# Kernel tuning notes

Measured on AMD Instinct MI355X. Metric: run time of the kernel, lower is better.

The kernel has to match this reference:

```python
import jax, jax.numpy as jnp
import numpy as np

H = 16        # num attention heads
KV = 4        # num key/value heads (GQA)
HD = 128      # head dim
CAP = 50.0    # attn_logits_soft_cap
SCALE = HD ** -0.5
ROPE_THETA = 10000.0


def rotate_half(x):
    return jnp.concatenate([-x[..., HD // 2:], x[..., :HD // 2]], axis=-1)


def setup_inputs() -> dict:
    key = jax.random.key(0)
    k0, k1, k2, k3, k4 = jax.random.split(key, 5)
    B, S, D = 2, 2048, 2048
    hidden_states = jax.random.normal(k0, (B, S, D), dtype=jnp.float32)
    # real rotary tables (HF apply_rotary_pos_emb convention: emb = cat(freqs, freqs))
    pos = jnp.arange(S, dtype=jnp.float32)
    inv_freq = 1.0 / (ROPE_THETA ** (jnp.arange(0, HD, 2, dtype=jnp.float32) / HD))
    freqs = pos[:, None] * inv_freq[None, :]          # [S, HD/2]
    emb = jnp.concatenate([freqs, freqs], axis=-1)    # [S, HD]
    cos = jnp.broadcast_to(jnp.cos(emb)[None], (B, S, HD)).astype(jnp.float32)
    sin = jnp.broadcast_to(jnp.sin(emb)[None], (B, S, HD)).astype(jnp.float32)
    Wq = 0.02 * jax.random.normal(k1, (H * HD, D), dtype=jnp.float32)
    Wk = 0.02 * jax.random.normal(k2, (KV * HD, D), dtype=jnp.float32)
    Wv = 0.02 * jax.random.normal(k3, (KV * HD, D), dtype=jnp.float32)
    Wo = 0.02 * jax.random.normal(k4, (D, H * HD), dtype=jnp.float32)
    return {"hidden_states": hidden_states, "cos": cos, "sin": sin,
            "Wq": Wq, "Wk": Wk, "Wv": Wv, "Wo": Wo}


def reference(hidden_states, cos, sin, Wq, Wk, Wv, Wo):
    B, S, D = hidden_states.shape
    # QKV projections (HF Linear: y = x @ W.T)
    q = jnp.einsum('bsd,hd->bsh', hidden_states, Wq).reshape(B, S, H, HD).transpose(0, 2, 1, 3)
    k = jnp.einsum('bsd,hd->bsh', hidden_states, Wk).reshape(B, S, KV, HD).transpose(0, 2, 1, 3)
    v = jnp.einsum('bsd,hd->bsh', hidden_states, Wv).reshape(B, S, KV, HD).transpose(0, 2, 1, 3)
    # RoPE
    cosb = cos[:, None, :, :]  # [B,1,S,HD]
    sinb = sin[:, None, :, :]
    q = q * cosb + rotate_half(q) * sinb
    k = k * cosb + rotate_half(k) * sinb
    # GQA: repeat kv heads
    rep = H // KV
    k = jnp.repeat(k, rep, axis=1)  # [B,H,S,HD]
    v = jnp.repeat(v, rep, axis=1)
    # splash attention == causal attention with tanh logits soft cap
    scores = jnp.einsum('bhqd,bhkd->bhqk', q * SCALE, k)
    scores = CAP * jnp.tanh(scores / CAP)
    causal = jnp.tril(jnp.ones((S, S), dtype=bool))
    scores = jnp.where(causal[None, None], scores, jnp.float32(-1e30))
    attn = jax.nn.softmax(scores, axis=-1)
    out = jnp.einsum('bhqk,bhkd->bhqd', attn, v)
    out = out.transpose(0, 2, 1, 3).reshape(B, S, H * HD)
    return jnp.einsum('bsh,dh->bsd', out, Wo)
```

## Files before the change

### kernel.cpp

```cpp
#include <hip/hip_runtime.h>
#include <hip/hip_bf16.h>
#include <stdint.h>

typedef __bf16 bf16x8 __attribute__((ext_vector_type(8)));
typedef float f32x4 __attribute__((ext_vector_type(4)));
typedef float f32x16 __attribute__((ext_vector_type(16)));

#define NB_H 16
#define NB_KV 4
#define NB_HD 128
#define NB_B 2
#define NB_S 2048
#define NB_D 2048
#define NB_M (NB_B*NB_S)
#define NB_NQKV 3072
#define CAPF 50.0f
#define SCALEF 0.08838834764831845f

__device__ __forceinline__ ushort f2bf(float x){
  uint32_t u = __float_as_uint(x);
  u += 0x7fffu + ((u >> 16) & 1u);
  return (ushort)(u >> 16);
}
__device__ __forceinline__ float bf2f(ushort u){
  return __uint_as_float(((uint32_t)u) << 16);
}
__device__ __forceinline__ void gload_lds16(const void* g, void* l){
  __builtin_amdgcn_global_load_lds(
      (const __attribute__((address_space(1))) uint32_t*)g,
      (__attribute__((address_space(3))) uint32_t*)l, 16, 0, 0);
}

__global__ __launch_bounds__(256) void cvt_all(const float* __restrict__ hs,
                                               const float* __restrict__ wq,
                                               const float* __restrict__ wk,
                                               const float* __restrict__ wv,
                                               const float* __restrict__ wo,
                                               ushort* __restrict__ hsb,
                                               ushort* __restrict__ wqkv,
                                               ushort* __restrict__ wob){
  int q = blockIdx.x * blockDim.x + threadIdx.x;
  const float* src; ushort* dst; int i;
  if (q < 2097152)      { src = hs; dst = hsb;            i = q; }
  else if (q < 3145728) { src = wq; dst = wqkv;           i = q - 2097152; }
  else if (q < 3407872) { src = wk; dst = wqkv + 4194304; i = q - 3145728; }
  else if (q < 3670016) { src = wv; dst = wqkv + 5242880; i = q - 3407872; }
  else                  { src = wo; dst = wob;            i = q - 3670016; }
  float4 v = ((const float4*)src)[i];
  ushort4 o;
  o.x = f2bf(v.x); o.y = f2bf(v.y); o.z = f2bf(v.z); o.w = f2bf(v.w);
  ((ushort4*)dst)[i] = o;
}

__global__ __launch_bounds__(256) void gemm_bt(const ushort* __restrict__ A,
                                               const ushort* __restrict__ Bw,
                                               ushort* __restrict__ Cb,
                                               float* __restrict__ Cf,
                                               int M, int N, int K, int nbx){
  int nwg = gridDim.x;
  int cpx = nwg >> 3;
  int wg = blockIdx.x;
  int swz = (wg & 7) * cpx + (wg >> 3);
  int bx = swz % nbx, by = swz / nbx;

  __shared__ ushort As[128 * 32];
  __shared__ ushort Bs[128 * 32];
  int tid = threadIdx.x;
  int w = tid >> 6, l = tid & 63;
  int lr = l & 15, lk = l >> 4;
  int row0 = by * 128, col0 = bx * 128;
  int wm = w >> 1, wn = w & 1;

  f32x4 acc[4][4];
#pragma unroll
  for (int mi = 0; mi < 4; ++mi)
#pragma unroll
    for (int nj = 0; nj < 4; ++nj)
      acc[mi][nj] = f32x4{0.f, 0.f, 0.f, 0.f};

  for (int k0 = 0; k0 < K; k0 += 32) {
#pragma unroll
    for (int c = 0; c < 2; ++c) {
      int off = w * 2048 + c * 1024 + l * 16;
      int r = off >> 6;
      int cb = off & 63;
      gload_lds16(A + (size_t)(row0 + r) * K + k0 + (cb >> 1), (char*)As + off);
      gload_lds16(Bw + (size_t)(col0 + r) * K + k0 + (cb >> 1), (char*)Bs + off);
    }
    __syncthreads();
    bf16x8 af[4], bfr[4];
#pragma unroll
    for (int mi = 0; mi < 4; ++mi)
      af[mi] = *(const bf16x8*)(As + (wm * 64 + mi * 16 + lr) * 32 + lk * 8);
#pragma unroll
    for (int nj = 0; nj < 4; ++nj)
      bfr[nj] = *(const bf16x8*)(Bs + (wn * 64 + nj * 16 + lr) * 32 + lk * 8);
    __builtin_amdgcn_s_setprio(1);
#pragma unroll
    for (int mi = 0; mi < 4; ++mi)
#pragma unroll
      for (int nj = 0; nj < 4; ++nj)
        acc[mi][nj] = __builtin_amdgcn_mfma_f32_16x16x32_bf16(af[mi], bfr[nj], acc[mi][nj], 0, 0, 0);
    __builtin_amdgcn_s_setprio(0);
    __syncthreads();
  }

#pragma unroll
  for (int mi = 0; mi < 4; ++mi)
#pragma unroll
    for (int nj = 0; nj < 4; ++nj)
#pragma unroll
      for (int i = 0; i < 4; ++i) {
        int r = row0 + wm * 64 + mi * 16 + lk * 4 + i;
        int c = col0 + wn * 64 + nj * 16 + lr;
        float v = acc[mi][nj][i];
        if (Cb) Cb[(size_t)r * N + c] = f2bf(v);
        else    Cf[(size_t)r * N + c] = v;
      }
}

__global__ __launch_bounds__(256) void rope_kernel(ushort* __restrict__ qkv,
                                                   const float* __restrict__ cosb,
                                                   const float* __restrict__ sinb){
  int idx = blockIdx.x * blockDim.x + threadIdx.x;
  if (idx >= NB_M * 20 * 64) return;
  int row = idx / 1280;
  int rem = idx - row * 1280;
  int head = rem >> 6;
  int d = rem & 63;
  size_t base = (size_t)row * NB_NQKV + head * 128 + d;
  float a = bf2f(qkv[base]);
  float b = bf2f(qkv[base + 64]);
  float c = cosb[row * 128 + d];
  float s = sinb[row * 128 + d];
  qkv[base]      = f2bf(a * c - b * s);
  qkv[base + 64] = f2bf(b * c + a * s);
}

__global__ __launch_bounds__(256) void vtrans_kernel(const ushort* __restrict__ qkv,
                                                     ushort* __restrict__ vt){
  __shared__ ushort tile[64 * 136];
  int bid = blockIdx.x;
  int s0 = (bid & 31) * 64;
  int kvh = (bid >> 5) & 3;
  int b = bid >> 7;
  int tid = threadIdx.x;
#pragma unroll
  for (int i = 0; i < 4; ++i) {
    int g = tid + i * 256;
    int r = g >> 4, c = g & 15;
    *(uint4*)(tile + r * 136 + c * 8) =
        *(const uint4*)(qkv + (size_t)(b * NB_S + s0 + r) * NB_NQKV + 2560 + kvh * 128 + c * 8);
  }
  __syncthreads();
#pragma unroll
  for (int i = 0; i < 4; ++i) {
    int g = tid + i * 256;
    int dd = g >> 3, c = g & 7;
    union { ushort u[8]; uint4 v; } tmp;
#pragma unroll
    for (int j = 0; j < 8; ++j) tmp.u[j] = tile[(c * 8 + j) * 136 + dd];
    *(uint4*)(vt + ((size_t)(b * NB_KV + kvh) * NB_HD + dd) * NB_S + s0 + c * 8) = tmp.v;
  }
}

__global__ __launch_bounds__(128, 4) void attn_kernel(const ushort* __restrict__ qkv,
                                                      const ushort* __restrict__ vt,
                                                      ushort* __restrict__ obuf){
  __shared__ float accbuf[4096];
  __shared__ float lbuf[64];
  __shared__ ushort trbuf[32 * 140];
  const int tid = threadIdx.x;
  const int w = tid >> 6, l = tid & 63;
  const int ql = l & 31, hi = l >> 5;
  const int blk = blockIdx.x;
  const int g = blk & 7;
  const int inner = blk >> 3;
  const int h_lo = inner & 3;
  const int qtile = 63 - (inner >> 2);
  const int b = g >> 2, kvh = g & 3;
  const int h = kvh * 4 + h_lo;
  const int q0 = qtile * 32;
  const int q = q0 + ql;
  const int nkt = (q0 + 95) >> 6;

  const ushort* Kg = qkv + (size_t)b * NB_S * NB_NQKV + 2048 + kvh * 128;
  const ushort* Vg = vt + (size_t)(b * NB_KV + kvh) * NB_HD * NB_S;

  bf16x8 qf[8];
  {
    const ushort* qrow = qkv + (size_t)(b * NB_S + q) * NB_NQKV + h * 128 + hi * 8;
#pragma unroll
    for (int dc = 0; dc < 8; ++dc)
      qf[dc] = *(const bf16x8*)(qrow + dc * 16);
  }

  f32x16 acc[4];
#pragma unroll
  for (int dt = 0; dt < 4; ++dt)
#pragma unroll
    for (int r = 0; r < 16; ++r) acc[dt][r] = 0.f;
  float l_run = 0.f;

  const float K1 = SCALEF / CAPF;
  const float KW = SCALEF * 1.4426950408889634f;

  for (int kt = w; kt < nkt; kt += 2) {
    const int s0 = kt * 64;
    f32x16 st[2];
#pragma unroll
    for (int t = 0; t < 2; ++t) {
#pragma unroll
      for (int r = 0; r < 16; ++r) st[t][r] = 0.f;
      const ushort* krow = Kg + (size_t)(s0 + t * 32 + ql) * NB_NQKV + hi * 8;
#pragma unroll
      for (int dc = 0; dc < 8; ++dc) {
        bf16x8 kf = *(const bf16x8*)(krow + dc * 16);
        st[t] = __builtin_amdgcn_mfma_f32_32x32x16_bf16(kf, qf[dc], st[t], 0, 0, 0);
      }
    }
    const bool full = (s0 + 63 <= q0);
    const int qmb = q - s0 - 4 * hi;
    float p[2][16];
    float rs = 0.f;
#pragma unroll
    for (int t = 0; t < 2; ++t)
#pragma unroll
      for (int r = 0; r < 16; ++r) {
        float s = st[t][r];
        float x = s * K1;
        float x2 = x * x;
        float ww = s * KW;
        float t1 = fmaf(x2, 0.13333334f, -0.33333334f);
        float y = fmaf(ww * x2, t1, ww);
        y = fminf(y, 72.134752f);
        if (!full) {
          const int koff = t * 32 + (r & 3) + 8 * (r >> 2);
          y = (koff <= qmb) ? y : -1e30f;
        }
        float pe = __builtin_amdgcn_exp2f(y);
        p[t][r] = pe;
        rs += pe;
      }
    rs += __shfl_xor(rs, 32);
    l_run += rs;
    union { __bf16 hh16[32]; uint u[16]; } Pk;
#pragma unroll
    for (int t = 0; t < 2; ++t)
#pragma unroll
      for (int r = 0; r < 16; ++r)
        Pk.hh16[t * 16 + r] = (__bf16)p[t][r];
    uint rec[2][2][2];
#pragma unroll
    for (int t = 0; t < 2; ++t)
#pragma unroll
      for (int hh = 0; hh < 2; ++hh)
#pragma unroll
        for (int wb = 0; wb < 2; ++wb) {
          uint send = hi ? Pk.u[t * 8 + 4 * hh + wb] : Pk.u[t * 8 + 4 * hh + 2 + wb];
          rec[t][hh][wb] = __shfl_xor(send, 32);
        }
#pragma unroll
    for (int c = 0; c < 4; ++c) {
      const int t = c >> 1, hh = c & 1;
      union { uint u[4]; bf16x8 v; } pf;
      pf.u[0] = hi ? rec[t][hh][0] : Pk.u[t * 8 + 4 * hh + 0];
      pf.u[1] = hi ? rec[t][hh][1] : Pk.u[t * 8 + 4 * hh + 1];
      pf.u[2] = hi ? Pk.u[t * 8 + 4 * hh + 2] : rec[t][hh][0];
      pf.u[3] = hi ? Pk.u[t * 8 + 4 * hh + 3] : rec[t][hh][1];
#pragma unroll
      for (int dt = 0; dt < 4; ++dt) {
        bf16x8 vf = *(const bf16x8*)(Vg + (size_t)(dt * 32 + ql) * NB_S + s0 + (c * 2 + hi) * 8);
        acc[dt] = __builtin_amdgcn_mfma_f32_32x32x16_bf16(vf, pf.v, acc[dt], 0, 0, 0);
      }
    }
  }

  if (w == 1) {
#pragma unroll
    for (int dt = 0; dt < 4; ++dt)
#pragma unroll
      for (int r = 0; r < 16; ++r)
        accbuf[(dt * 16 + r) * 64 + l] = acc[dt][r];
    lbuf[l] = l_run;
  }
  __syncthreads();
  if (w == 0) {
#pragma unroll
    for (int dt = 0; dt < 4; ++dt)
#pragma unroll
      for (int r = 0; r < 16; ++r)
        acc[dt][r] += accbuf[(dt * 16 + r) * 64 + l];
    l_run += lbuf[l];
    const float inv = __builtin_amdgcn_rcpf(l_run);
#pragma unroll
    for (int dt = 0; dt < 4; ++dt)
#pragma unroll
      for (int gg = 0; gg < 4; ++gg) {
        ushort4 o;
        o.x = f2bf(acc[dt][4 * gg + 0] * inv);
        o.y = f2bf(acc[dt][4 * gg + 1] * inv);
        o.z = f2bf(acc[dt][4 * gg + 2] * inv);
        o.w = f2bf(acc[dt][4 * gg + 3] * inv);
        const int d0 = dt * 32 + gg * 8 + hi * 4;
        *(ushort4*)(trbuf + ql * 140 + d0) = o;
      }
  }
  __syncthreads();
#pragma unroll
  for (int i = 0; i < 4; ++i) {
    const int qr = i * 8 + (tid >> 4);
    const int c = tid & 15;
    uint4 v = *(const uint4*)(trbuf + qr * 140 + c * 8);
    *(uint4*)(obuf + (size_t)(b * NB_S + q0 + qr) * NB_D + h * 128 + c * 8) = v;
  }
}

extern "C" void kernel_launch(void* const* d_in, const int* in_sizes, int n_in,
                              void* d_out, int out_size, void* d_ws, size_t ws_size,
                              hipStream_t stream) {
  const float* hs   = (const float*)d_in[0];
  const float* cosb = (const float*)d_in[1];
  const float* sinb = (const float*)d_in[2];
  const float* Wq   = (const float*)d_in[3];
  const float* Wk   = (const float*)d_in[4];
  const float* Wv   = (const float*)d_in[5];
  const float* Wo   = (const float*)d_in[6];
  float* out = (float*)d_out;
  char* ws = (char*)d_ws;

  ushort* hsb  = (ushort*)(ws + 0);
  ushort* wqkv = (ushort*)(ws + 16777216);
  ushort* wob  = (ushort*)(ws + 29360128);
  ushort* qkvb = (ushort*)(ws + 37748736);
  ushort* vtb  = (ushort*)(ws + 62914560);
  ushort* ob   = (ushort*)(ws + 67108864);

  cvt_all<<<18432, 256, 0, stream>>>(hs, Wq, Wk, Wv, Wo, hsb, wqkv, wob);

  gemm_bt<<<768, 256, 0, stream>>>(hsb, wqkv, qkvb, nullptr, NB_M, NB_NQKV, NB_D, 24);
  rope_kernel<<<(NB_M * 20 * 64 + 255) / 256, 256, 0, stream>>>(qkvb, cosb, sinb);
  vtrans_kernel<<<NB_B * NB_KV * (NB_S / 64), 256, 0, stream>>>(qkvb, vtb);

  attn_kernel<<<2048, 128, 0, stream>>>(qkvb, vtb, ob);

  gemm_bt<<<512, 256, 0, stream>>>(ob, wob, nullptr, out, NB_M, NB_D, NB_D, 16);
}
```

Baseline: 427.2 us.

## Fuse RoPE into K/V fragment repack and Q load; halve attention LDS reduction buffer

Replaces the separate RoPE and V-transpose kernels with one kv_repack kernel. It applies RoPE to K and writes K and V in MFMA-fragment order, so each lane in attention does contiguous 16-byte loads at a fixed stride. RoPE for Q now runs inside the attention kernel when Q is loaded, which removes the full read-modify-write pass over Q. The cross-wave accumulator reduction now goes through half-size LDS in two rounds, which should help occupancy but adds syncs. The s_setprio hints around the GEMM MFMAs are also removed, and the V fragment buffer reuses the hidden-state workspace region.

```diff
diff --git a/kernel.cpp b/kernel.cpp
--- a/kernel.cpp
+++ b/kernel.cpp
@@ -95,13 +95,11 @@
 #pragma unroll
     for (int nj = 0; nj < 4; ++nj)
       bfr[nj] = *(const bf16x8*)(Bs + (wn * 64 + nj * 16 + lr) * 32 + lk * 8);
-    __builtin_amdgcn_s_setprio(1);
 #pragma unroll
     for (int mi = 0; mi < 4; ++mi)
 #pragma unroll
       for (int nj = 0; nj < 4; ++nj)
         acc[mi][nj] = __builtin_amdgcn_mfma_f32_16x16x32_bf16(af[mi], bfr[nj], acc[mi][nj], 0, 0, 0);
-    __builtin_amdgcn_s_setprio(0);
     __syncthreads();
   }
 
@@ -119,55 +117,70 @@
       }
 }
 
-__global__ __launch_bounds__(256) void rope_kernel(ushort* __restrict__ qkv,
-                                                   const float* __restrict__ cosb,
-                                                   const float* __restrict__ sinb){
-  int idx = blockIdx.x * blockDim.x + threadIdx.x;
-  if (idx >= NB_M * 20 * 64) return;
-  int row = idx / 1280;
-  int rem = idx - row * 1280;
-  int head = rem >> 6;
-  int d = rem & 63;
-  size_t base = (size_t)row * NB_NQKV + head * 128 + d;
-  float a = bf2f(qkv[base]);
-  float b = bf2f(qkv[base + 64]);
-  float c = cosb[row * 128 + d];
-  float s = sinb[row * 128 + d];
-  qkv[base]      = f2bf(a * c - b * s);
-  qkv[base + 64] = f2bf(b * c + a * s);
-}
-
-__global__ __launch_bounds__(256) void vtrans_kernel(const ushort* __restrict__ qkv,
-                                                     ushort* __restrict__ vt){
-  __shared__ ushort tile[64 * 136];
-  int bid = blockIdx.x;
-  int s0 = (bid & 31) * 64;
-  int kvh = (bid >> 5) & 3;
-  int b = bid >> 7;
-  int tid = threadIdx.x;
+__global__ __launch_bounds__(256) void kv_repack(const ushort* __restrict__ qkv,
+                                                 const float* __restrict__ cosb,
+                                                 const float* __restrict__ sinb,
+                                                 ushort* __restrict__ Kf,
+                                                 ushort* __restrict__ Vf){
+  __shared__ ushort Ks[64 * 136];
+  __shared__ ushort Vs[64 * 136];
+  const int blk = blockIdx.x;
+  const int kt = blk & 31, kvh = (blk >> 5) & 3, b = blk >> 7;
+  const int s0 = kt * 64;
+  const int tid = threadIdx.x;
+  {
+    const int r = tid >> 2, c0 = tid & 3;
+    const ushort* src = qkv + (size_t)(b * NB_S + s0 + r) * NB_NQKV + kvh * 128;
+#pragma unroll
+    for (int k = 0; k < 4; ++k) {
+      int c = c0 + k * 4;
+      *(uint4*)(Ks + r * 136 + c * 8) = *(const uint4*)(src + 2048 + c * 8);
+      *(uint4*)(Vs + r * 136 + c * 8) = *(const uint4*)(src + 2560 + c * 8);
+    }
+  }
+  __syncthreads();
+  const int w = tid >> 6, l = tid & 63, ql = l & 31, hi = l >> 5;
+  const size_t fbase = (size_t)((b * NB_KV + kvh) * 32 + kt) * 8192;
 #pragma unroll
   for (int i = 0; i < 4; ++i) {
-    int g = tid + i * 256;
-    int r = g >> 4, c = g & 15;
-    *(uint4*)(tile + r * 136 + c * 8) =
-        *(const uint4*)(qkv + (size_t)(b * NB_S + s0 + r) * NB_NQKV + 2560 + kvh * 128 + c * 8);
-  }
-  __syncthreads();
+    const int idx = i * 4 + w;
+    const int t = idx >> 3, dc = idx & 7;
+    const int row = t * 32 + ql;
+    const int d0 = dc * 16 + hi * 8;
+    union { ushort u[8]; uint4 v; } a, p2;
+    a.v  = *(const uint4*)(Ks + row * 136 + d0);
+    p2.v = *(const uint4*)(Ks + row * 136 + (d0 ^ 64));
+    const float* cr = cosb + (size_t)(b * NB_S + s0 + row) * 128 + d0;
+    const float* sr = sinb + (size_t)(b * NB_S + s0 + row) * 128 + d0;
+    const float sgn = (dc < 4) ? -1.f : 1.f;
+    ushort outv[8];
+#pragma unroll
+    for (int j2 = 0; j2 < 8; ++j2) {
+      float kv = bf2f(a.u[j2]), pv = bf2f(p2.u[j2]);
+      outv[j2] = f2bf(fmaf(sgn * pv, sr[j2], kv * cr[j2]));
+    }
+    *(uint4*)(Kf + fbase + ((size_t)idx * 64 + l) * 8) = *(const uint4*)outv;
+  }
 #pragma unroll
   for (int i = 0; i < 4; ++i) {
-    int g = tid + i * 256;
-    int dd = g >> 3, c = g & 7;
-    union { ushort u[8]; uint4 v; } tmp;
-#pragma unroll
-    for (int j = 0; j < 8; ++j) tmp.u[j] = tile[(c * 8 + j) * 136 + dd];
-    *(uint4*)(vt + ((size_t)(b * NB_KV + kvh) * NB_HD + dd) * NB_S + s0 + c * 8) = tmp.v;
+    const int idx = i * 4 + w;
+    const int c = idx >> 2, dt = idx & 3;
+    const int col = dt * 32 + ql;
+    ushort outv[8];
+#pragma unroll
+    for (int j2 = 0; j2 < 8; ++j2)
+      outv[j2] = Vs[((2 * c + hi) * 8 + j2) * 136 + col];
+    *(uint4*)(Vf + fbase + ((size_t)idx * 64 + l) * 8) = *(const uint4*)outv;
   }
 }
 
 __global__ __launch_bounds__(128, 4) void attn_kernel(const ushort* __restrict__ qkv,
-                                                      const ushort* __restrict__ vt,
+                                                      const ushort* __restrict__ Kf,
+                                                      const ushort* __restrict__ Vf,
+                                                      const float* __restrict__ cosb,
+                                                      const float* __restrict__ sinb,
                                                       ushort* __restrict__ obuf){
-  __shared__ float accbuf[4096];
+  __shared__ float accbuf[2048];
   __shared__ float lbuf[64];
   __shared__ ushort trbuf[32 * 140];
   const int tid = threadIdx.x;
@@ -184,15 +197,30 @@
   const int q = q0 + ql;
   const int nkt = (q0 + 95) >> 6;
 
-  const ushort* Kg = qkv + (size_t)b * NB_S * NB_NQKV + 2048 + kvh * 128;
-  const ushort* Vg = vt + (size_t)(b * NB_KV + kvh) * NB_HD * NB_S;
+  const ushort* Kfb = Kf + (size_t)(b * NB_KV + kvh) * 262144 + l * 8;
+  const ushort* Vfb = Vf + (size_t)(b * NB_KV + kvh) * 262144 + l * 8;
 
   bf16x8 qf[8];
   {
-    const ushort* qrow = qkv + (size_t)(b * NB_S + q) * NB_NQKV + h * 128 + hi * 8;
-#pragma unroll
-    for (int dc = 0; dc < 8; ++dc)
-      qf[dc] = *(const bf16x8*)(qrow + dc * 16);
+    const ushort* qrow = qkv + (size_t)(b * NB_S + q) * NB_NQKV + h * 128;
+    const float* cr = cosb + (size_t)(b * NB_S + q) * 128;
+    const float* sr = sinb + (size_t)(b * NB_S + q) * 128;
+#pragma unroll
+    for (int dc = 0; dc < 4; ++dc) {
+      union { ushort u[8]; uint4 v; } lo, hi8;
+      lo.v  = *(const uint4*)(qrow + dc * 16 + hi * 8);
+      hi8.v = *(const uint4*)(qrow + (dc + 4) * 16 + hi * 8);
+      __bf16 o1[8], o2[8];
+#pragma unroll
+      for (int j2 = 0; j2 < 8; ++j2) {
+        const int d1 = dc * 16 + hi * 8 + j2;
+        float a = bf2f(lo.u[j2]), bb = bf2f(hi8.u[j2]);
+        o1[j2] = (__bf16)(a * cr[d1] - bb * sr[d1]);
+        o2[j2] = (__bf16)(bb * cr[d1 + 64] + a * sr[d1 + 64]);
+      }
+      qf[dc]     = *(bf16x8*)o1;
+      qf[dc + 4] = *(bf16x8*)o2;
+    }
   }
 
   f32x16 acc[4];
@@ -207,15 +235,16 @@
 
   for (int kt = w; kt < nkt; kt += 2) {
     const int s0 = kt * 64;
+    const ushort* kp = Kfb + (size_t)kt * 8192;
+    const ushort* vp = Vfb + (size_t)kt * 8192;
     f32x16 st[2];
 #pragma unroll
     for (int t = 0; t < 2; ++t) {
 #pragma unroll
       for (int r = 0; r < 16; ++r) st[t][r] = 0.f;
-      const ushort* krow = Kg + (size_t)(s0 + t * 32 + ql) * NB_NQKV + hi * 8;
 #pragma unroll
       for (int dc = 0; dc < 8; ++dc) {
-        bf16x8 kf = *(const bf16x8*)(krow + dc * 16);
+        bf16x8 kf = *(const bf16x8*)(kp + (t * 8 + dc) * 512);
         st[t] = __builtin_amdgcn_mfma_f32_32x32x16_bf16(kf, qf[dc], st[t], 0, 0, 0);
       }
     }
@@ -270,7 +299,7 @@
       pf.u[3] = hi ? Pk.u[t * 8 + 4 * hh + 3] : rec[t][hh][1];
 #pragma unroll
       for (int dt = 0; dt < 4; ++dt) {
-        bf16x8 vf = *(const bf16x8*)(Vg + (size_t)(dt * 32 + ql) * NB_S + s0 + (c * 2 + hi) * 8);
+        bf16x8 vf = *(const bf16x8*)(vp + (c * 4 + dt) * 512);
         acc[dt] = __builtin_amdgcn_mfma_f32_32x32x16_bf16(vf, pf.v, acc[dt], 0, 0, 0);
       }
     }
@@ -278,7 +307,7 @@
 
   if (w == 1) {
 #pragma unroll
-    for (int dt = 0; dt < 4; ++dt)
+    for (int dt = 0; dt < 2; ++dt)
 #pragma unroll
       for (int r = 0; r < 16; ++r)
         accbuf[(dt * 16 + r) * 64 + l] = acc[dt][r];
@@ -287,11 +316,27 @@
   __syncthreads();
   if (w == 0) {
 #pragma unroll
-    for (int dt = 0; dt < 4; ++dt)
+    for (int dt = 0; dt < 2; ++dt)
 #pragma unroll
       for (int r = 0; r < 16; ++r)
         acc[dt][r] += accbuf[(dt * 16 + r) * 64 + l];
     l_run += lbuf[l];
+  }
+  __syncthreads();
+  if (w == 1) {
+#pragma unroll
+    for (int dt = 0; dt < 2; ++dt)
+#pragma unroll
+      for (int r = 0; r < 16; ++r)
+        accbuf[(dt * 16 + r) * 64 + l] = acc[dt + 2][r];
+  }
+  __syncthreads();
+  if (w == 0) {
+#pragma unroll
+    for (int dt = 0; dt < 2; ++dt)
+#pragma unroll
+      for (int r = 0; r < 16; ++r)
+        acc[dt + 2][r] += accbuf[(dt * 16 + r) * 64 + l];
     const float inv = __builtin_amdgcn_rcpf(l_run);
 #pragma unroll
     for (int dt = 0; dt < 4; ++dt)
@@ -333,16 +378,17 @@
   ushort* wqkv = (ushort*)(ws + 16777216);
   ushort* wob  = (ushort*)(ws + 29360128);
   ushort* qkvb = (ushort*)(ws + 37748736);
-  ushort* vtb  = (ushort*)(ws + 62914560);
+  ushort* kfb  = (ushort*)(ws + 62914560);
   ushort* ob   = (ushort*)(ws + 67108864);
+  ushort* vfb  = (ushort*)(ws + 0);
 
   cvt_all<<<18432, 256, 0, stream>>>(hs, Wq, Wk, Wv, Wo, hsb, wqkv, wob);
 
   gemm_bt<<<768, 256, 0, stream>>>(hsb, wqkv, qkvb, nullptr, NB_M, NB_NQKV, NB_D, 24);
-  rope_kernel<<<(NB_M * 20 * 64 + 255) / 256, 256, 0, stream>>>(qkvb, cosb, sinb);
-  vtrans_kernel<<<NB_B * NB_KV * (NB_S / 64), 256, 0, stream>>>(qkvb, vtb);
-
-  attn_kernel<<<2048, 128, 0, stream>>>(qkvb, vtb, ob);
+
+  kv_repack<<<256, 256, 0, stream>>>(qkvb, cosb, sinb, kfb, vfb);
+
+  attn_kernel<<<2048, 128, 0, stream>>>(qkvb, kfb, vfb, cosb, sinb, ob);
 
   gemm_bt<<<512, 256, 0, stream>>>(ob, wob, nullptr, out, NB_M, NB_D, NB_D, 16);
 }
```

New measurement: 481.7 us. +12.8%, slower.
